# Optimization experiments

Hardware: AMD Instinct MI355X
Metric: run time of the kernel (lower is better)

## Reference

```python
import jax, jax.numpy as jnp
import numpy as np

B, D, H, W = 16, 256, 32, 32
K = 4096
LIM = 3 ** 0.5  # codebook init range from the module


def setup_inputs() -> dict:
    key = jax.random.key(0)
    kx, kc = jax.random.split(key)
    x = jax.random.normal(kx, (B, D, H, W), dtype=jnp.float32)
    codebook = jax.random.uniform(kc, (K, D), dtype=jnp.float32) * LIM
    return {"x": x, "codebook": codebook}


def reference(x, codebook):
    # x: [B, D, H, W] -> flat tokens [B*H*W, D]
    b, d, h, w = x.shape
    flat = jnp.transpose(x, (0, 2, 3, 1)).reshape(-1, d)
    # Squared Euclidean distances (argmin identical to cdist p=2 argmin):
    # ||a||^2 - 2 a.b + ||b||^2
    d2 = (
        jnp.sum(flat * flat, axis=-1, keepdims=True)
        - 2.0 * flat @ codebook.T
        + jnp.sum(codebook * codebook, axis=-1)
    )  # [N, K]
    idx = jnp.argmin(d2, axis=1)  # [N]
    quantized = codebook[idx]  # gather, [N, D]
    quantized = quantized.reshape(b, h, w, d)
    return jnp.transpose(quantized, (0, 3, 1, 2))  # [B, D, H, W]
```

## Files before the change

kernel.cpp:

```cpp
#include <hip/hip_runtime.h>
#include <math.h>

#define DD    256
#define HWD   1024
#define NTOK  16384
#define KK    4096

typedef __attribute__((ext_vector_type(8))) short     bf16x8;
typedef __attribute__((ext_vector_type(4))) float     f32x4;
typedef __attribute__((ext_vector_type(8))) unsigned short ushort8;

__device__ __forceinline__ unsigned short f2bf(float f) {
    unsigned u = __float_as_uint(f);
    unsigned r = (u + 0x7FFFu + ((u >> 16) & 1u)) >> 16;
    return (unsigned short)r;
}
__device__ __forceinline__ float bf2f(unsigned short h) {
    return __uint_as_float(((unsigned)h) << 16);
}

#define GLOAD16(gaddr, laddr)                                                   \
    __builtin_amdgcn_global_load_lds(                                           \
        (const __attribute__((address_space(1))) unsigned int*)(gaddr),         \
        (__attribute__((address_space(3))) unsigned int*)(laddr), 16, 0, 0)

__global__ __launch_bounds__(256) void vq_splitx(const float* __restrict__ x,
                                                 unsigned short* __restrict__ Ax) {
    const int blk = blockIdx.x;
    const int tid = threadIdx.x;
    const int b = blk >> 4;
    const int hw0 = (blk & 15) << 6;

    __shared__ float xls[DD * 64];

    const float* xb = x + (size_t)b * (DD * HWD) + hw0;
    #pragma unroll 8
    for (int it = 0; it < 64; ++it) {
        int e = it * 256 + tid;
        int d = e >> 6, i = e & 63;
        xls[d * 64 + i] = xb[d * HWD + i];
    }
    __syncthreads();

    const int tok_l = tid >> 2;
    const int part  = tid & 3;
    const int n = b * HWD + hw0 + tok_l;
    unsigned short* dst = Ax + (size_t)n * 768 + part * 192;

    #pragma unroll
    for (int c8 = 0; c8 < 8; ++c8) {
        const int dbase = part * 64 + c8 * 8;
        ushort8 w0, w1, w2;
        #pragma unroll
        for (int q = 0; q < 8; ++q) {
            float v = xls[(dbase + q) * 64 + tok_l];
            unsigned short hq = f2bf(v);
            unsigned short lq = f2bf(v - bf2f(hq));
            const int i0 = 3 * q, i1 = 3 * q + 1, i2 = 3 * q + 2;
            if (i0 < 8) w0[i0] = hq; else if (i0 < 16) w1[i0 - 8] = hq; else w2[i0 - 16] = hq;
            if (i1 < 8) w0[i1] = lq; else if (i1 < 16) w1[i1 - 8] = lq; else w2[i1 - 16] = lq;
            if (i2 < 8) w0[i2] = hq; else if (i2 < 16) w1[i2 - 8] = hq; else w2[i2 - 16] = hq;
        }
        *(ushort8*)(dst + c8 * 24)      = w0;
        *(ushort8*)(dst + c8 * 24 + 8)  = w1;
        *(ushort8*)(dst + c8 * 24 + 16) = w2;
    }
}

__global__ __launch_bounds__(256) void vq_splitc(const float* __restrict__ cb,
                                                 unsigned short* __restrict__ Bc) {
    const int gid = blockIdx.x * 256 + threadIdx.x;
    const int k = gid >> 5;
    const int j = gid & 31;
    const float4* cb4 = (const float4*)cb;
    float4 a = cb4[k * 64 + j * 2];
    float4 bq = cb4[k * 64 + j * 2 + 1];
    float vv[8] = {a.x, a.y, a.z, a.w, bq.x, bq.y, bq.z, bq.w};
    ushort8 w0, w1, w2;
    #pragma unroll
    for (int q = 0; q < 8; ++q) {
        unsigned short hq = f2bf(vv[q]);
        unsigned short lq = f2bf(vv[q] - bf2f(hq));
        const int i0 = 3 * q, i1 = 3 * q + 1, i2 = 3 * q + 2;
        if (i0 < 8) w0[i0] = hq; else if (i0 < 16) w1[i0 - 8] = hq; else w2[i0 - 16] = hq;
        if (i1 < 8) w0[i1] = hq; else if (i1 < 16) w1[i1 - 8] = hq; else w2[i1 - 16] = hq;
        if (i2 < 8) w0[i2] = lq; else if (i2 < 16) w1[i2 - 8] = lq; else w2[i2 - 16] = lq;
    }
    unsigned short* dst = Bc + (size_t)k * 768 + j * 24;
    *(ushort8*)(dst)      = w0;
    *(ushort8*)(dst + 8)  = w1;
    *(ushort8*)(dst + 16) = w2;
}

__global__ __launch_bounds__(256) void vq_transpose(const float* __restrict__ cb,
                                                    float* __restrict__ cbT) {
    __shared__ float t[32][33];
    const int kt = blockIdx.x * 32, dt = blockIdx.y * 32;
    const int tx = threadIdx.x & 31, ty = threadIdx.x >> 5;
    #pragma unroll
    for (int r = 0; r < 32; r += 8)
        t[ty + r][tx] = cb[(kt + ty + r) * DD + dt + tx];
    __syncthreads();
    #pragma unroll
    for (int r = 0; r < 32; r += 8)
        cbT[(size_t)(dt + ty + r) * KK + kt + tx] = t[tx][ty + r];
}

__global__ __launch_bounds__(256) void vq_cnorm(const float* __restrict__ cb,
                                                float* __restrict__ cnorm) {
    int k = (blockIdx.x * 256 + threadIdx.x) >> 6;
    int lane = threadIdx.x & 63;
    float4 v = reinterpret_cast<const float4*>(cb)[k * 64 + lane];
    float s = v.x * v.x + v.y * v.y + v.z * v.z + v.w * v.w;
    #pragma unroll
    for (int off = 32; off > 0; off >>= 1) s += __shfl_xor(s, off, 64);
    if (lane == 0) cnorm[k] = s;
}

__global__ void vq_zero(int* cnt) { if (threadIdx.x == 0) *cnt = 0; }

#define BN 128
#define BK 64
#define KRED 768
#define NPH 4
#define MARGIN 0.05f

__device__ __forceinline__ void stage_ab(const unsigned short* __restrict__ Ax,
                                         const unsigned short* __restrict__ Bc,
                                         unsigned short* AsF, unsigned short* BsF,
                                         int buf, int mblk, int phase, int nt, int kk,
                                         int wid, int lane) {
    const int L3  = lane >> 3;
    const int gsw = (lane & 7) ^ L3;
    #pragma unroll
    for (int ib = 0; ib < 4; ++ib) {
        const int rb = wid * 32 + ib * 8;
        const int ldsoff = __builtin_amdgcn_readfirstlane(buf * 8192 + rb * 64);
        GLOAD16(Ax + (size_t)(mblk * 128 + rb + L3) * KRED + kk * 64 + gsw * 8,
                AsF + ldsoff);
        GLOAD16(Bc + (size_t)(phase * 1024 + nt * 128 + rb + L3) * KRED + kk * 64 + gsw * 8,
                BsF + ldsoff);
    }
}

__global__ __launch_bounds__(256, 2) void vq_gemm_min(
    const unsigned short* __restrict__ Ax,
    const unsigned short* __restrict__ Bc,
    const float* __restrict__ cnorm,
    float* __restrict__ candb, float* __restrict__ cands, int* __restrict__ candk)
{
    const int tid  = threadIdx.x;
    const int wid  = tid >> 6, lane = tid & 63;
    const int wm   = wid >> 1, wn = wid & 1;
    const int l15  = lane & 15, l4 = lane >> 4;
    const int mblk = blockIdx.x;
    const int phase = blockIdx.y;

    __shared__ alignas(16) unsigned short As[2 * 128 * BK];
    __shared__ alignas(16) unsigned short Bs[2 * 128 * BK];
    __shared__ float mrg[128][2][3];

    float runb[16], runs[16];
    int   runk[16];
    #pragma unroll
    for (int e = 0; e < 16; ++e) { runb[e] = 3.0e38f; runs[e] = 3.0e38f; runk[e] = 0; }

    f32x4 acc[4][4];
    #pragma unroll
    for (int mi = 0; mi < 4; ++mi)
        #pragma unroll
        for (int ni = 0; ni < 4; ++ni)
            acc[mi][ni] = (f32x4){0.f, 0.f, 0.f, 0.f};

    stage_ab(Ax, Bc, As, Bs, 0, mblk, phase, 0, 0, wid, lane);

    int cur = 0;
    for (int t = 0; t < 96; ++t) {
        const int nt = t / 12, kk = t - nt * 12;
        if (t < 95) {
            const int t1 = t + 1;
            const int nt1 = t1 / 12, kk1 = t1 - nt1 * 12;
            stage_ab(Ax, Bc, As, Bs, cur ^ 1, mblk, phase, nt1, kk1, wid, lane);
            asm volatile("s_waitcnt vmcnt(8)" ::: "memory");
        } else {
            asm volatile("s_waitcnt vmcnt(0)" ::: "memory");
        }
        __builtin_amdgcn_s_barrier();

        __builtin_amdgcn_s_setprio(1);
        #pragma unroll
        for (int kh = 0; kh < 2; ++kh) {
            bf16x8 af[4], bfr[4];
            const int cxor = ((kh * 4 + l4) ^ (l15 & 7)) << 3;
            #pragma unroll
            for (int mi = 0; mi < 4; ++mi) {
                const int r = wm * 64 + mi * 16 + l15;
                af[mi] = *(const bf16x8*)&As[cur * 8192 + r * 64 + cxor];
            }
            #pragma unroll
            for (int ni = 0; ni < 4; ++ni) {
                const int c = wn * 64 + ni * 16 + l15;
                bfr[ni] = *(const bf16x8*)&Bs[cur * 8192 + c * 64 + cxor];
            }
            #pragma unroll
            for (int mi = 0; mi < 4; ++mi)
                #pragma unroll
                for (int ni = 0; ni < 4; ++ni)
                    acc[mi][ni] = __builtin_amdgcn_mfma_f32_16x16x32_bf16(
                        af[mi], bfr[ni], acc[mi][ni], 0, 0, 0);
        }
        __builtin_amdgcn_s_setprio(0);

        if (kk == 11) {
            #pragma unroll
            for (int ni = 0; ni < 4; ++ni) {
                const int c = phase * 1024 + nt * BN + wn * 64 + ni * 16 + l15;
                const float cn = cnorm[c];
                #pragma unroll
                for (int mi = 0; mi < 4; ++mi) {
                    #pragma unroll
                    for (int rg = 0; rg < 4; ++rg) {
                        float d = fmaf(-2.0f, acc[mi][ni][rg], cn);
                        const int e = mi * 4 + rg;
                        float ob = runb[e];
                        runs[e] = fminf(fmaxf(d, ob), runs[e]);
                        runk[e] = (d < ob) ? c : runk[e];
                        runb[e] = fminf(d, ob);
                    }
                    acc[mi][ni] = (f32x4){0.f, 0.f, 0.f, 0.f};
                }
            }
        }
        __builtin_amdgcn_s_barrier();
        cur ^= 1;
    }

    #pragma unroll
    for (int e = 0; e < 16; ++e) {
        float b = runb[e], s = runs[e];
        int   k = runk[e];
        #pragma unroll
        for (int off = 1; off < 16; off <<= 1) {
            float ob = __shfl_xor(b, off, 64);
            float os = __shfl_xor(s, off, 64);
            int   ok = __shfl_xor(k, off, 64);
            float nb = fminf(b, ob);
            s = fminf(fminf(s, os), fmaxf(b, ob));
            k = (ob < b) ? ok : k;
            b = nb;
        }
        if (l15 == 0) {
            int row = wm * 64 + (e >> 2) * 16 + l4 * 4 + (e & 3);
            mrg[row][wn][0] = b;
            mrg[row][wn][1] = s;
            mrg[row][wn][2] = __int_as_float(k);
        }
    }
    __syncthreads();

    if (tid < 128) {
        const int row = tid;
        float b0 = mrg[row][0][0], s0 = mrg[row][0][1];
        float b1 = mrg[row][1][0], s1 = mrg[row][1][1];
        int   k0 = __float_as_int(mrg[row][0][2]);
        int   k1 = __float_as_int(mrg[row][1][2]);
        float b = fminf(b0, b1);
        float s = fminf(fminf(s0, s1), fmaxf(b0, b1));
        int   k = (b1 < b0) ? k1 : k0;
        const int tok = mblk * 128 + row;
        candb[phase * NTOK + tok] = b;
        cands[phase * NTOK + tok] = s;
        candk[phase * NTOK + tok] = k;
    }
}

__global__ __launch_bounds__(256) void vq_merge(
    const float* __restrict__ candb, const float* __restrict__ cands,
    const int* __restrict__ candk, int* __restrict__ out_k,
    int* __restrict__ flagged, int* __restrict__ cnt,
    unsigned long long* __restrict__ packed)
{
    const int tok = blockIdx.x * 256 + threadIdx.x;
    float b = candb[tok], s = cands[tok];
    int   k = candk[tok];
    #pragma unroll
    for (int p = 1; p < NPH; ++p) {
        float pb = candb[p * NTOK + tok], ps = cands[p * NTOK + tok];
        int   pk = candk[p * NTOK + tok];
        float nb = fminf(b, pb);
        s = fminf(fminf(s, ps), fmaxf(b, pb));
        k = (pb < b) ? pk : k;
        b = nb;
    }
    out_k[tok] = k;
    if (s - b < MARGIN) {
        int i = atomicAdd(cnt, 1);
        flagged[i] = tok;
        packed[i] = 0xFFFFFFFFFFFFFFFFull;
    }
}

__global__ __launch_bounds__(256) void vq_exact(
    const float* __restrict__ x, const float* __restrict__ cbT,
    const float* __restrict__ cnorm, const int* __restrict__ flagged,
    const int* __restrict__ cnt, unsigned long long* __restrict__ packed)
{
    const int tid = threadIdx.x;
    const int lane = tid & 63, wid = tid >> 6;
    const int items = (*cnt) << 2;
    __shared__ float xs[DD];
    __shared__ unsigned long long wbest[4];

    for (int w = blockIdx.x; w < items; w += gridDim.x) {
        const int ti = w >> 2;
        const int ch = w & 3;
        const int tok = flagged[ti];
        const int b = tok >> 10, hw = tok & 1023;
        __syncthreads();
        xs[tid] = x[(size_t)b * (DD * HWD) + tid * HWD + hw];
        __syncthreads();

        const int kbase = ch * 1024 + tid * 4;
        float a0 = 0.f, a1 = 0.f, a2 = 0.f, a3 = 0.f;
        #pragma unroll 8
        for (int d = 0; d < DD; ++d) {
            const float xv = xs[d];
            const float4 cv = *(const float4*)(cbT + (size_t)d * KK + kbase);
            a0 = fmaf(xv, cv.x, a0);
            a1 = fmaf(xv, cv.y, a1);
            a2 = fmaf(xv, cv.z, a2);
            a3 = fmaf(xv, cv.w, a3);
        }
        float d0 = fmaf(-2.f, a0, cnorm[kbase]);
        float d1 = fmaf(-2.f, a1, cnorm[kbase + 1]);
        float d2 = fmaf(-2.f, a2, cnorm[kbase + 2]);
        float d3 = fmaf(-2.f, a3, cnorm[kbase + 3]);
        float best = d0; int bk = kbase;
        if (d1 < best) { best = d1; bk = kbase + 1; }
        if (d2 < best) { best = d2; bk = kbase + 2; }
        if (d3 < best) { best = d3; bk = kbase + 3; }
        unsigned ub = __float_as_uint(best);
        ub = (ub & 0x80000000u) ? ~ub : (ub | 0x80000000u);
        unsigned long long pk = ((unsigned long long)ub << 32) | (unsigned)bk;
        #pragma unroll
        for (int off = 1; off < 64; off <<= 1) {
            unsigned long long o = __shfl_xor(pk, off, 64);
            pk = (o < pk) ? o : pk;
        }
        if (lane == 0) wbest[wid] = pk;
        __syncthreads();
        if (tid == 0) {
            unsigned long long m = wbest[0];
            #pragma unroll
            for (int i = 1; i < 4; ++i) m = (wbest[i] < m) ? wbest[i] : m;
            atomicMin(&packed[ti], m);
        }
    }
}

__global__ __launch_bounds__(256) void vq_unpack(
    const int* __restrict__ flagged, const int* __restrict__ cnt,
    const unsigned long long* __restrict__ packed, int* __restrict__ out_k)
{
    const int i = blockIdx.x * 256 + threadIdx.x;
    if (i < *cnt) out_k[flagged[i]] = (int)(packed[i] & 0xFFFFFFFFull);
}

__global__ __launch_bounds__(256) void vq_gather(const float* __restrict__ cb,
                                                 const int* __restrict__ out_k,
                                                 float* __restrict__ out) {
    const int blk = blockIdx.x;
    const int tid = threadIdx.x;
    const int b = blk >> 4;
    const int hw0 = (blk & 15) << 6;

    __shared__ int   bks[64];
    __shared__ float ts[64][65];

    if (tid < 64) bks[tid] = out_k[blk * 64 + tid];
    __syncthreads();

    const int rr = tid >> 6;
    const int j  = tid & 63;
    float* ob = out + (size_t)b * (DD * HWD) + hw0;
    #pragma unroll
    for (int c = 0; c < 4; ++c) {
        const int d0 = c << 6;
        #pragma unroll 4
        for (int it = 0; it < 16; ++it) {
            int tok = it * 4 + rr;
            ts[tok][j] = cb[bks[tok] * DD + d0 + j];
        }
        __syncthreads();
        #pragma unroll 4
        for (int it = 0; it < 16; ++it) {
            int dl = it * 4 + rr;
            ob[(d0 + dl) * HWD + j] = ts[j][dl];
        }
        __syncthreads();
    }
}

#define TT2   64
#define KGRP2 16
#define NW2   16
__global__ __launch_bounds__(1024, 8) void vq_dist2(const float* __restrict__ x,
                                                    const float* __restrict__ cbT,
                                                    const float* __restrict__ cnorm,
                                                    float* __restrict__ cand_d,
                                                    int* __restrict__ cand_k) {
    const int blk = blockIdx.x;
    const int phase = blockIdx.y;
    const int tid = threadIdx.x;
    const int wid = tid >> 6, lane = tid & 63;
    const int b = blk >> 4;
    const int hw0 = (blk & 15) << 6;

    __shared__ alignas(16) float xs[DD * TT2];
    __shared__ float bd_s[NW2][TT2];
    __shared__ int   bk_s[NW2][TT2];

    const float* xb = x + (size_t)b * (DD * HWD) + hw0;
    #pragma unroll
    for (int it = 0; it < 16; ++it) {
        int e = it * 1024 + tid;
        int d = e >> 6, i = e & 63;
        xs[(d >> 1) * 128 + i * 2 + (d & 1)] = xb[d * HWD + i];
    }
    __syncthreads();

    const float2* xs2 = reinterpret_cast<const float2*>(xs) + lane;
    float best = 3.0e38f;
    int bestk = 0;
    const int g0 = phase * 128 + wid * 8;
    for (int j = 0; j < 8; ++j) {
        const int k0 = __builtin_amdgcn_readfirstlane((g0 + j) * KGRP2);
        const float* __restrict__ cT0 = cbT + k0;
        const float* __restrict__ cn0 = cnorm + k0;
        float acc[KGRP2];
        #pragma unroll
        for (int t = 0; t < KGRP2; ++t) acc[t] = 0.f;
        #pragma unroll 4
        for (int d2 = 0; d2 < DD / 2; ++d2) {
            float2 xv = xs2[d2 * 64];
            const float* __restrict__ cA = cT0 + (size_t)(2 * d2) * KK;
            const float* __restrict__ cB = cA + KK;
            #pragma unroll
            for (int t = 0; t < KGRP2; ++t) acc[t] = fmaf(xv.x, cA[t], acc[t]);
            #pragma unroll
            for (int t = 0; t < KGRP2; ++t) acc[t] = fmaf(xv.y, cB[t], acc[t]);
        }
        #pragma unroll
        for (int t = 0; t < KGRP2; ++t) {
            float dv = fmaf(-2.0f, acc[t], cn0[t]);
            if (dv < best) { best = dv; bestk = k0 + t; }
        }
    }
    bd_s[wid][lane] = best;
    bk_s[wid][lane] = bestk;
    __syncthreads();
    if (tid < TT2) {
        float bdv = bd_s[0][lane];
        int   bkv = bk_s[0][lane];
        #pragma unroll
        for (int w = 1; w < NW2; ++w) {
            float ddv = bd_s[w][lane];
            int   kw = bk_s[w][lane];
            if (ddv < bdv || (ddv == bdv && kw < bkv)) { bdv = ddv; bkv = kw; }
        }
        int nn = blk * TT2 + lane;
        cand_d[phase * NTOK + nn] = bdv;
        cand_k[phase * NTOK + nn] = bkv;
    }
}

__global__ __launch_bounds__(256) void vq_merge2(const float* __restrict__ cand_d,
                                                 const int* __restrict__ cand_k,
                                                 int* __restrict__ out_k) {
    const int tok = blockIdx.x * 256 + threadIdx.x;
    float d0 = cand_d[tok]; int k0 = cand_k[tok];
    float d1 = cand_d[NTOK + tok]; int k1 = cand_k[NTOK + tok];
    out_k[tok] = (d1 < d0 || (d1 == d0 && k1 < k0)) ? k1 : k0;
}

extern "C" void kernel_launch(void* const* d_in, const int* in_sizes, int n_in,
                              void* d_out, int out_size, void* d_ws, size_t ws_size,
                              hipStream_t stream) {
    const float* x  = (const float*)d_in[0];
    const float* cb = (const float*)d_in[1];
    float* out = (float*)d_out;

    char* w = (char*)d_ws;
    float* cbT    = (float*)(w);
    float* cnorm  = (float*)(w + 4194304);
    int*   out_k  = (int*)  (w + 4210688);
    int*   cnt    = (int*)  (w + 4276224);
    int*   flagged= (int*)  (w + 4276480);
    float* candb  = (float*)(w + 4342016);
    float* cands  = (float*)(w + 4866304);
    int*   candk  = (int*)  (w + 5390592);
    unsigned long long* packed = (unsigned long long*)(w + 5914880);
    unsigned short* Ax = (unsigned short*)(w + 6045952);
    unsigned short* Bc = (unsigned short*)(w + 31211776);
    const size_t BIG_NEED = 37503232;

    vq_transpose<<<dim3(KK / 32, DD / 32), dim3(256), 0, stream>>>(cb, cbT);
    vq_cnorm<<<dim3(KK / 4), dim3(256), 0, stream>>>(cb, cnorm);

    if (ws_size >= BIG_NEED) {
        vq_splitx<<<dim3(256), dim3(256), 0, stream>>>(x, Ax);
        vq_splitc<<<dim3(512), dim3(256), 0, stream>>>(cb, Bc);
        vq_zero<<<dim3(1), dim3(64), 0, stream>>>(cnt);
        vq_gemm_min<<<dim3(NTOK / 128, NPH), dim3(256), 0, stream>>>(
            Ax, Bc, cnorm, candb, cands, candk);
        vq_merge<<<dim3(NTOK / 256), dim3(256), 0, stream>>>(
            candb, cands, candk, out_k, flagged, cnt, packed);
        vq_exact<<<dim3(1024), dim3(256), 0, stream>>>(
            x, cbT, cnorm, flagged, cnt, packed);
        vq_unpack<<<dim3(NTOK / 256), dim3(256), 0, stream>>>(
            flagged, cnt, packed, out_k);
    } else {
        float* cand_d = candb;
        int*   cand_k = candk;
        vq_dist2<<<dim3(NTOK / TT2, 2), dim3(1024), 0, stream>>>(
            x, cbT, cnorm, cand_d, cand_k);
        vq_merge2<<<dim3(NTOK / 256), dim3(256), 0, stream>>>(cand_d, cand_k, out_k);
    }
    vq_gather<<<dim3(NTOK / 64), dim3(256), 0, stream>>>(cb, out_k, out);
}
```

Before: 248.0 us.

## Raise GEMM occupancy with single-buffered LDS, per-tile LDS merge, and fused codebook prep

The distance GEMM now splits the codebook into 8 phases instead of 4 and asks for 4 blocks per CU instead of 2. To fit that, it uses single-buffered LDS and merges each column tile's per-row min and second-min into shared memory, so the running per-row registers go away. The codebook transpose and bf16 split are fused into one kernel that reads the codebook once through LDS. The zero kernel is replaced by a memset. The trade-off is that the previous global-to-LDS prefetch overlap is lost, since each step now waits on its own load between two barriers, and the merge code does more shuffles and LDS writes per tile.

New measurement: 266.4 us. 1.07x slower.

```diff
diff --git a/kernel.cpp b/kernel.cpp
--- a/kernel.cpp
+++ b/kernel.cpp
@@ -67,29 +67,50 @@
     }
 }
 
-__global__ __launch_bounds__(256) void vq_splitc(const float* __restrict__ cb,
-                                                 unsigned short* __restrict__ Bc) {
-    const int gid = blockIdx.x * 256 + threadIdx.x;
-    const int k = gid >> 5;
-    const int j = gid & 31;
-    const float4* cb4 = (const float4*)cb;
-    float4 a = cb4[k * 64 + j * 2];
-    float4 bq = cb4[k * 64 + j * 2 + 1];
-    float vv[8] = {a.x, a.y, a.z, a.w, bq.x, bq.y, bq.z, bq.w};
-    ushort8 w0, w1, w2;
-    #pragma unroll
-    for (int q = 0; q < 8; ++q) {
-        unsigned short hq = f2bf(vv[q]);
-        unsigned short lq = f2bf(vv[q] - bf2f(hq));
-        const int i0 = 3 * q, i1 = 3 * q + 1, i2 = 3 * q + 2;
-        if (i0 < 8) w0[i0] = hq; else if (i0 < 16) w1[i0 - 8] = hq; else w2[i0 - 16] = hq;
-        if (i1 < 8) w0[i1] = hq; else if (i1 < 16) w1[i1 - 8] = hq; else w2[i1 - 16] = hq;
-        if (i2 < 8) w0[i2] = lq; else if (i2 < 16) w1[i2 - 8] = lq; else w2[i2 - 16] = lq;
-    }
-    unsigned short* dst = Bc + (size_t)k * 768 + j * 24;
-    *(ushort8*)(dst)      = w0;
-    *(ushort8*)(dst + 8)  = w1;
-    *(ushort8*)(dst + 16) = w2;
+__global__ __launch_bounds__(256) void vq_prepc(const float* __restrict__ cb,
+                                                float* __restrict__ cbT,
+                                                unsigned short* __restrict__ Bc) {
+    __shared__ float cbl[32 * 260];
+    const int tid = threadIdx.x;
+    const int k0 = blockIdx.x * 32;
+
+    #pragma unroll
+    for (int it = 0; it < 32; ++it) {
+        int e = it * 256 + tid;
+        int r = e >> 8, c = e & 255;
+        cbl[r * 260 + c] = cb[(size_t)(k0 + r) * DD + c];
+    }
+    __syncthreads();
+
+    {
+        const int kk = tid & 31, d0 = tid >> 5;
+        for (int dd = d0; dd < DD; dd += 8)
+            cbT[(size_t)dd * KK + k0 + kk] = cbl[kk * 260 + dd];
+    }
+
+    #pragma unroll
+    for (int it = 0; it < 4; ++it) {
+        const int item = it * 256 + tid;
+        const int kl = item >> 5, j = item & 31;
+        const float* src = &cbl[kl * 260 + j * 8];
+        float vv[8];
+        #pragma unroll
+        for (int q = 0; q < 8; ++q) vv[q] = src[q];
+        ushort8 w0, w1, w2;
+        #pragma unroll
+        for (int q = 0; q < 8; ++q) {
+            unsigned short hq = f2bf(vv[q]);
+            unsigned short lq = f2bf(vv[q] - bf2f(hq));
+            const int i0 = 3 * q, i1 = 3 * q + 1, i2 = 3 * q + 2;
+            if (i0 < 8) w0[i0] = hq; else if (i0 < 16) w1[i0 - 8] = hq; else w2[i0 - 16] = hq;
+            if (i1 < 8) w0[i1] = hq; else if (i1 < 16) w1[i1 - 8] = hq; else w2[i1 - 16] = hq;
+            if (i2 < 8) w0[i2] = lq; else if (i2 < 16) w1[i2 - 8] = lq; else w2[i2 - 16] = lq;
+        }
+        unsigned short* dst = Bc + (size_t)(k0 + kl) * 768 + j * 24;
+        *(ushort8*)(dst)      = w0;
+        *(ushort8*)(dst + 8)  = w1;
+        *(ushort8*)(dst + 16) = w2;
+    }
 }
 
 __global__ __launch_bounds__(256) void vq_transpose(const float* __restrict__ cb,
@@ -117,33 +138,31 @@
     if (lane == 0) cnorm[k] = s;
 }
 
-__global__ void vq_zero(int* cnt) { if (threadIdx.x == 0) *cnt = 0; }
-
 #define BN 128
 #define BK 64
 #define KRED 768
-#define NPH 4
+#define NPH 8
 #define MARGIN 0.05f
 
 __device__ __forceinline__ void stage_ab(const unsigned short* __restrict__ Ax,
                                          const unsigned short* __restrict__ Bc,
                                          unsigned short* AsF, unsigned short* BsF,
-                                         int buf, int mblk, int phase, int nt, int kk,
+                                         int mblk, int phase, int nt, int kk,
                                          int wid, int lane) {
     const int L3  = lane >> 3;
     const int gsw = (lane & 7) ^ L3;
     #pragma unroll
     for (int ib = 0; ib < 4; ++ib) {
         const int rb = wid * 32 + ib * 8;
-        const int ldsoff = __builtin_amdgcn_readfirstlane(buf * 8192 + rb * 64);
+        const int ldsoff = __builtin_amdgcn_readfirstlane(rb * 64);
         GLOAD16(Ax + (size_t)(mblk * 128 + rb + L3) * KRED + kk * 64 + gsw * 8,
                 AsF + ldsoff);
-        GLOAD16(Bc + (size_t)(phase * 1024 + nt * 128 + rb + L3) * KRED + kk * 64 + gsw * 8,
+        GLOAD16(Bc + (size_t)(phase * 512 + nt * 128 + rb + L3) * KRED + kk * 64 + gsw * 8,
                 BsF + ldsoff);
     }
 }
 
-__global__ __launch_bounds__(256, 2) void vq_gemm_min(
+__global__ __launch_bounds__(256, 4) void vq_gemm_min(
     const unsigned short* __restrict__ Ax,
     const unsigned short* __restrict__ Bc,
     const float* __restrict__ cnorm,
@@ -156,14 +175,16 @@
     const int mblk = blockIdx.x;
     const int phase = blockIdx.y;
 
-    __shared__ alignas(16) unsigned short As[2 * 128 * BK];
-    __shared__ alignas(16) unsigned short Bs[2 * 128 * BK];
+    __shared__ alignas(16) unsigned short As[128 * BK];
+    __shared__ alignas(16) unsigned short Bs[128 * BK];
     __shared__ float mrg[128][2][3];
 
-    float runb[16], runs[16];
-    int   runk[16];
-    #pragma unroll
-    for (int e = 0; e < 16; ++e) { runb[e] = 3.0e38f; runs[e] = 3.0e38f; runk[e] = 0; }
+    {
+        const int row = tid >> 1, w = tid & 1;
+        mrg[row][w][0] = 3.0e38f;
+        mrg[row][w][1] = 3.0e38f;
+        mrg[row][w][2] = __int_as_float(0);
+    }
 
     f32x4 acc[4][4];
     #pragma unroll
@@ -172,20 +193,11 @@
         for (int ni = 0; ni < 4; ++ni)
             acc[mi][ni] = (f32x4){0.f, 0.f, 0.f, 0.f};
 
-    stage_ab(Ax, Bc, As, Bs, 0, mblk, phase, 0, 0, wid, lane);
-
-    int cur = 0;
-    for (int t = 0; t < 96; ++t) {
+    for (int t = 0; t < 48; ++t) {
         const int nt = t / 12, kk = t - nt * 12;
-        if (t < 95) {
-            const int t1 = t + 1;
-            const int nt1 = t1 / 12, kk1 = t1 - nt1 * 12;
-            stage_ab(Ax, Bc, As, Bs, cur ^ 1, mblk, phase, nt1, kk1, wid, lane);
-            asm volatile("s_waitcnt vmcnt(8)" ::: "memory");
-        } else {
-            asm volatile("s_waitcnt vmcnt(0)" ::: "memory");
-        }
-        __builtin_amdgcn_s_barrier();
+        __syncthreads();
+        stage_ab(Ax, Bc, As, Bs, mblk, phase, nt, kk, wid, lane);
+        __syncthreads();
 
         __builtin_amdgcn_s_setprio(1);
         #pragma unroll
@@ -195,12 +207,12 @@
             #pragma unroll
             for (int mi = 0; mi < 4; ++mi) {
                 const int r = wm * 64 + mi * 16 + l15;
-                af[mi] = *(const bf16x8*)&As[cur * 8192 + r * 64 + cxor];
+                af[mi] = *(const bf16x8*)&As[r * 64 + cxor];
             }
             #pragma unroll
             for (int ni = 0; ni < 4; ++ni) {
                 const int c = wn * 64 + ni * 16 + l15;
-                bfr[ni] = *(const bf16x8*)&Bs[cur * 8192 + c * 64 + cxor];
+                bfr[ni] = *(const bf16x8*)&Bs[c * 64 + cxor];
             }
             #pragma unroll
             for (int mi = 0; mi < 4; ++mi)
@@ -212,48 +224,49 @@
         __builtin_amdgcn_s_setprio(0);
 
         if (kk == 11) {
-            #pragma unroll
-            for (int ni = 0; ni < 4; ++ni) {
-                const int c = phase * 1024 + nt * BN + wn * 64 + ni * 16 + l15;
-                const float cn = cnorm[c];
+            float cn[4];
+            #pragma unroll
+            for (int ni = 0; ni < 4; ++ni)
+                cn[ni] = cnorm[phase * 512 + nt * BN + wn * 64 + ni * 16 + l15];
+
+            #pragma unroll
+            for (int mi = 0; mi < 4; ++mi) {
                 #pragma unroll
-                for (int mi = 0; mi < 4; ++mi) {
+                for (int rg = 0; rg < 4; ++rg) {
+                    float b = 3.0e38f, s = 3.0e38f;
+                    int   k = 0;
                     #pragma unroll
-                    for (int rg = 0; rg < 4; ++rg) {
-                        float d = fmaf(-2.0f, acc[mi][ni][rg], cn);
-                        const int e = mi * 4 + rg;
-                        float ob = runb[e];
-                        runs[e] = fminf(fmaxf(d, ob), runs[e]);
-                        runk[e] = (d < ob) ? c : runk[e];
-                        runb[e] = fminf(d, ob);
+                    for (int ni = 0; ni < 4; ++ni) {
+                        const int c = phase * 512 + nt * BN + wn * 64 + ni * 16 + l15;
+                        float d = fmaf(-2.0f, acc[mi][ni][rg], cn[ni]);
+                        float ob = b;
+                        s = fminf(fmaxf(d, ob), s);
+                        k = (d < ob) ? c : k;
+                        b = fminf(d, ob);
                     }
+                    #pragma unroll
+                    for (int off = 1; off < 16; off <<= 1) {
+                        float obv = __shfl_xor(b, off, 64);
+                        float osv = __shfl_xor(s, off, 64);
+                        int   okv = __shfl_xor(k, off, 64);
+                        s = fminf(fminf(s, osv), fmaxf(b, obv));
+                        k = (obv < b) ? okv : k;
+                        b = fminf(b, obv);
+                    }
+                    if (l15 == 0) {
+                        const int row = wm * 64 + mi * 16 + l4 * 4 + rg;
+                        float ob0 = mrg[row][wn][0], os0 = mrg[row][wn][1];
+                        int   ok0 = __float_as_int(mrg[row][wn][2]);
+                        float ns = fminf(fminf(os0, s), fmaxf(ob0, b));
+                        mrg[row][wn][0] = fminf(ob0, b);
+                        mrg[row][wn][1] = ns;
+                        mrg[row][wn][2] = __int_as_float((b < ob0) ? k : ok0);
+                    }
+                }
+                #pragma unroll
+                for (int ni = 0; ni < 4; ++ni)
                     acc[mi][ni] = (f32x4){0.f, 0.f, 0.f, 0.f};
-                }
             }
-        }
-        __builtin_amdgcn_s_barrier();
-        cur ^= 1;
-    }
-
-    #pragma unroll
-    for (int e = 0; e < 16; ++e) {
-        float b = runb[e], s = runs[e];
-        int   k = runk[e];
-        #pragma unroll
-        for (int off = 1; off < 16; off <<= 1) {
-            float ob = __shfl_xor(b, off, 64);
-            float os = __shfl_xor(s, off, 64);
-            int   ok = __shfl_xor(k, off, 64);
-            float nb = fminf(b, ob);
-            s = fminf(fminf(s, os), fmaxf(b, ob));
-            k = (ob < b) ? ok : k;
-            b = nb;
-        }
-        if (l15 == 0) {
-            int row = wm * 64 + (e >> 2) * 16 + l4 * 4 + (e & 3);
-            mrg[row][wn][0] = b;
-            mrg[row][wn][1] = s;
-            mrg[row][wn][2] = __int_as_float(k);
         }
     }
     __syncthreads();
@@ -504,13 +517,11 @@
     unsigned short* Bc = (unsigned short*)(w + 31211776);
     const size_t BIG_NEED = 37503232;
 
-    vq_transpose<<<dim3(KK / 32, DD / 32), dim3(256), 0, stream>>>(cb, cbT);
-    vq_cnorm<<<dim3(KK / 4), dim3(256), 0, stream>>>(cb, cnorm);
-
     if (ws_size >= BIG_NEED) {
+        vq_prepc<<<dim3(KK / 32), dim3(256), 0, stream>>>(cb, cbT, Bc);
+        vq_cnorm<<<dim3(KK / 4), dim3(256), 0, stream>>>(cb, cnorm);
         vq_splitx<<<dim3(256), dim3(256), 0, stream>>>(x, Ax);
-        vq_splitc<<<dim3(512), dim3(256), 0, stream>>>(cb, Bc);
-        vq_zero<<<dim3(1), dim3(64), 0, stream>>>(cnt);
+        hipMemsetAsync(cnt, 0, sizeof(int), stream);
         vq_gemm_min<<<dim3(NTOK / 128, NPH), dim3(256), 0, stream>>>(
             Ax, Bc, cnorm, candb, cands, candk);
         vq_merge<<<dim3(NTOK / 256), dim3(256), 0, stream>>>(
@@ -520,6 +531,8 @@
         vq_unpack<<<dim3(NTOK / 256), dim3(256), 0, stream>>>(
             flagged, cnt, packed, out_k);
     } else {
+        vq_transpose<<<dim3(KK / 32, DD / 32), dim3(256), 0, stream>>>(cb, cbT);
+        vq_cnorm<<<dim3(KK / 4), dim3(256), 0, stream>>>(cb, cnorm);
         float* cand_d = candb;
         int*   cand_k = candk;
         vq_dist2<<<dim3(NTOK / TT2, 2), dim3(1024), 0, stream>>>(
```
